# Performance work log

Measured on AMD Instinct MI355X. Metric: run time of the kernel, lower is better.

## Reference

```python
import jax, jax.numpy as jnp
import numpy as np
import math

EMBED = 1024
FF = 4096
HEADS = 16
HEAD = EMBED // HEADS
EPS = 1e-5


def new_gelu(x):
    c = math.sqrt(2.0 / math.pi)
    return 0.5 * x * (1.0 + jnp.tanh(c * (x + 0.044715 * x ** 3)))


def layer_norm(x, g, b):
    mu = jnp.mean(x, axis=-1, keepdims=True)
    var = jnp.var(x, axis=-1, keepdims=True)
    return (x - mu) * jax.lax.rsqrt(var + EPS) * g + b


def setup_inputs() -> dict:
    key = jax.random.key(0)
    ks = jax.random.split(key, 16)
    s = 0.02
    d = {
        'x': jax.random.normal(ks[0], (2, 2048, EMBED), jnp.float32),
        'Wq': jax.random.normal(ks[1], (EMBED, EMBED)) * s,
        'bq': jnp.zeros((EMBED,)),
        'Wk': jax.random.normal(ks[2], (EMBED, EMBED)) * s,
        'bk': jnp.zeros((EMBED,)),
        'Wv': jax.random.normal(ks[3], (EMBED, EMBED)) * s,
        'bv': jnp.zeros((EMBED,)),
        'Wp': jax.random.normal(ks[4], (EMBED, EMBED)) * s,
        'bp': jnp.zeros((EMBED,)),
        'W1': jax.random.normal(ks[5], (EMBED, FF)) * s,
        'b1': jnp.zeros((FF,)),
        'W2': jax.random.normal(ks[6], (FF, EMBED)) * s,
        'b2': jnp.zeros((EMBED,)),
        'g1': jnp.ones((EMBED,)), 'be1': jnp.zeros((EMBED,)),
        'g2': jnp.ones((EMBED,)), 'be2': jnp.zeros((EMBED,)),
    }
    return d


def reference(x, Wq, bq, Wk, bk, Wv, bv, Wp, bp, W1, b1, W2, b2, g1, be1, g2, be2):
    B, S, D = x.shape
    h = layer_norm(x, g1, be1)
    # project and split heads: [B,S,D] -> [B,H,S,Hd]
    def heads(y):
        return y.reshape(B, S, HEADS, HEAD).transpose(0, 2, 1, 3)
    Q = heads(h @ Wq + bq)
    K = heads(h @ Wk + bk)
    V = heads(h @ Wv + bv)
    att = jnp.einsum('bhqd,bhkd->bhqk', Q, K) / math.sqrt(HEAD)
    att = jax.nn.softmax(att, axis=-1)
    out = jnp.einsum('bhqk,bhkd->bhqd', att, V)
    out = out.transpose(0, 2, 1, 3).reshape(B, S, D)
    x = x + (out @ Wp + bp)  # dropout p=0 / eval -> identity
    h2 = layer_norm(x, g2, be2)
    x = x + (new_gelu(h2 @ W1 + b1) @ W2 + b2)
    return x
```

## Files before the change

### kernel.cpp

```cpp
#include <hip/hip_runtime.h>
#include <cstdint>


typedef __attribute__((ext_vector_type(8))) short short8;
typedef __attribute__((ext_vector_type(4))) float f32x4;

__device__ __forceinline__ float bf2f(unsigned short u) {
    union { unsigned int i; float f; } v; v.i = ((unsigned int)u) << 16; return v.f;
}
__device__ __forceinline__ unsigned short f2bf(float f) {
    union { float f; unsigned int i; } v; v.f = f;
    unsigned int u = v.i;
    u += 0x7fff + ((u >> 16) & 1);
    return (unsigned short)(u >> 16);
}
__device__ __forceinline__ float gelu_f(float x) {
    float u = 0.7978845608028654f * (x + 0.044715f * x * x * x);
    float t = 1.f - 2.f / (__expf(2.f * u) + 1.f);
    return 0.5f * x * (1.f + t);
}
__device__ __forceinline__ void async16(const unsigned short* gp, unsigned short* lp) {
    __builtin_amdgcn_global_load_lds(
        (__attribute__((address_space(1))) void*)(gp),
        (__attribute__((address_space(3))) void*)(lp),
        16, 0, 0);
}

__device__ __forceinline__ void ln_dev(
    const float* __restrict__ x, const float* __restrict__ g,
    const float* __restrict__ b, unsigned short* __restrict__ o,
    int row, float* red)
{
    const int tid = threadIdx.x;
    const float4 v = ((const float4*)(x + (size_t)row * 1024))[tid];
    float f0 = v.x, f1 = v.y, f2 = v.z, f3 = v.w;
    float sum = f0 + f1 + f2 + f3;
    float sq  = f0 * f0 + f1 * f1 + f2 * f2 + f3 * f3;
    for (int off = 1; off < 64; off <<= 1) {
        sum += __shfl_xor(sum, off);
        sq  += __shfl_xor(sq,  off);
    }
    int wv = tid >> 6, ln = tid & 63;
    if (ln == 0) { red[wv] = sum; red[4 + wv] = sq; }
    __syncthreads();
    sum = red[0] + red[1] + red[2] + red[3];
    sq  = red[4] + red[5] + red[6] + red[7];
    float mu  = sum * (1.0f / 1024.0f);
    float var = sq  * (1.0f / 1024.0f) - mu * mu;
    float rsd = rsqrtf(fmaxf(var, 0.f) + 1e-5f);
    const float4 gg = ((const float4*)g)[tid];
    const float4 bb = ((const float4*)b)[tid];
    unsigned short* orow = o + (size_t)row * 1024;
    orow[4 * tid + 0] = f2bf((f0 - mu) * rsd * gg.x + bb.x);
    orow[4 * tid + 1] = f2bf((f1 - mu) * rsd * gg.y + bb.y);
    orow[4 * tid + 2] = f2bf((f2 - mu) * rsd * gg.z + bb.z);
    orow[4 * tid + 3] = f2bf((f3 - mu) * rsd * gg.w + bb.w);
}

__device__ __forceinline__ void transpose_dev(
    const float* __restrict__ in, unsigned short* __restrict__ out,
    int R, int C, int inStride, int bx, int by, unsigned short* tile )
{
    const int tx = threadIdx.x & 15, ty = threadIdx.x >> 4;
    const int c0 = bx * 64, r0 = by * 64;
#pragma unroll
    for (int i = 0; i < 4; ++i) {
        int r = ty + 16 * i;
        float4 v = *(const float4*)(in + (size_t)(r0 + r) * inStride + c0 + tx * 4);
        tile[r * 70 + tx * 4 + 0] = f2bf(v.x);
        tile[r * 70 + tx * 4 + 1] = f2bf(v.y);
        tile[r * 70 + tx * 4 + 2] = f2bf(v.z);
        tile[r * 70 + tx * 4 + 3] = f2bf(v.w);
    }
    __syncthreads();
#pragma unroll
    for (int i = 0; i < 4; ++i) {
        int c = ty * 4 + i;
        ushort4 o;
        o.x = tile[(tx * 4 + 0) * 70 + c];
        o.y = tile[(tx * 4 + 1) * 70 + c];
        o.z = tile[(tx * 4 + 2) * 70 + c];
        o.w = tile[(tx * 4 + 3) * 70 + c];
        *(ushort4*)(out + (size_t)(c0 + c) * R + r0 + tx * 4) = o;
    }
}

__global__ __launch_bounds__(256) void ln_k(
    const float* __restrict__ x, const float* __restrict__ g,
    const float* __restrict__ b, unsigned short* __restrict__ o)
{
    __shared__ float red[8];
    ln_dev(x, g, b, o, blockIdx.x, red);
}
__global__ __launch_bounds__(256) void transpose_f2b(
    const float* __restrict__ in, unsigned short* __restrict__ out,
    int R, int C, int inStride)
{
    __shared__ unsigned short tile[64 * 70];
    transpose_dev(in, out, R, C, inStride, blockIdx.x, blockIdx.y, tile);
}
__global__ __launch_bounds__(256) void bcat_k(
    const float* __restrict__ a, const float* __restrict__ b,
    const float* __restrict__ c, float* __restrict__ dst)
{
    int i = blockIdx.x * 256 + threadIdx.x;
    float v = (i < 1024) ? a[i] : (i < 2048) ? b[i - 1024] : c[i - 2048];
    dst[i] = v;
}

__global__ __launch_bounds__(256) void prep1_k(
    const float* __restrict__ x,
    const float* __restrict__ g1, const float* __restrict__ be1,
    const float* __restrict__ Wq, const float* __restrict__ Wk,
    const float* __restrict__ Wv,
    const float* __restrict__ bq, const float* __restrict__ bk,
    const float* __restrict__ bv,
    unsigned short* __restrict__ hb,
    unsigned short* __restrict__ WTqkv,
    float* __restrict__ bcat)
{
    __shared__ unsigned short smem[64 * 70];
    const int b = blockIdx.x;
    if (b < 4096) {
        ln_dev(x, g1, be1, hb, b, (float*)smem);
    } else if (b < 4096 + 768) {
        int t = b - 4096;
        int w = t >> 8;
        int tt = t & 255;
        const float* W = (w == 0) ? Wq : (w == 1) ? Wk : Wv;
        transpose_dev(W, WTqkv + (size_t)w * 1024 * 1024,
                      1024, 1024, 1024, tt & 15, tt >> 4, smem);
    } else {
        int i = (b - 4096 - 768) * 256 + threadIdx.x;
        float v = (i < 1024) ? bq[i] : (i < 2048) ? bk[i - 1024] : bv[i - 2048];
        bcat[i] = v;
    }
}

__global__ __launch_bounds__(256) void prep2_k(
    const float* __restrict__ x1,
    const float* __restrict__ g2, const float* __restrict__ be2,
    const float* __restrict__ W1, const float* __restrict__ W2,
    unsigned short* __restrict__ h2,
    unsigned short* __restrict__ WT1,
    unsigned short* __restrict__ WT2)
{
    __shared__ unsigned short smem[64 * 70];
    const int b = blockIdx.x;
    if (b < 4096) {
        ln_dev(x1, g2, be2, h2, b, (float*)smem);
    } else if (b < 4096 + 1024) {
        int t = b - 4096;
        transpose_dev(W1, WT1, 1024, 4096, 4096, t & 63, t >> 6, smem);
    } else {
        int t = b - 4096 - 1024;
        transpose_dev(W2, WT2, 4096, 1024, 1024, t & 15, t >> 4, smem);
    }
}

__global__ __launch_bounds__(256) void vt_k(
    const unsigned short* __restrict__ src, int stride,
    unsigned short* __restrict__ Vt)
{
    __shared__ unsigned short tile[64][70];
    const int tx = threadIdx.x & 15, ty = threadIdx.x >> 4;
    const int t0 = blockIdx.x * 64;
    const int bh = blockIdx.y;
    const int bo = (bh >> 4) * 2048;
    const int ho = (bh & 15) * 64;
    const unsigned short* s = src + (size_t)bo * stride + ho;
#pragma unroll
    for (int i = 0; i < 4; ++i) {
        int r = ty + 16 * i;
        ushort4 v = *(const ushort4*)(s + (size_t)(t0 + r) * stride + tx * 4);
        tile[r][tx * 4 + 0] = v.x;
        tile[r][tx * 4 + 1] = v.y;
        tile[r][tx * 4 + 2] = v.z;
        tile[r][tx * 4 + 3] = v.w;
    }
    __syncthreads();
    unsigned short* dst = Vt + (size_t)bh * 64 * 2048;
#pragma unroll
    for (int i = 0; i < 4; ++i) {
        int d = ty * 4 + i;
        ushort4 o;
        o.x = tile[tx * 4 + 0][d];
        o.y = tile[tx * 4 + 1][d];
        o.z = tile[tx * 4 + 2][d];
        o.w = tile[tx * 4 + 3][d];
        *(ushort4*)(dst + (size_t)d * 2048 + t0 + tx * 4) = o;
    }
}

__global__ __launch_bounds__(256, 2) void gemm_bt(
    const unsigned short* __restrict__ A,
    const unsigned short* __restrict__ Bt,
    const float* __restrict__ bias,
    const float* __restrict__ res,
    void* __restrict__ C,
    int M, int N, int K, int ldb, int dogelu, int out32)
{
    __shared__ unsigned short sA[2 * 128 * 32];
    __shared__ unsigned short sB[2 * 128 * 32];
    const int tid  = threadIdx.x;
    const int wave = tid >> 6;
    const int lane = tid & 63;
    const int quad = lane >> 4;
    const int l15  = lane & 15;
    const int bm = blockIdx.y * 128;
    const int bn = blockIdx.x * 128;
    const int wM = (wave >> 1) * 64;
    const int wN = (wave & 1) * 64;

    f32x4 acc[4][4];
#pragma unroll
    for (int i = 0; i < 4; ++i)
#pragma unroll
        for (int j = 0; j < 4; ++j)
            acc[i][j] = (f32x4){0.f, 0.f, 0.f, 0.f};

    const int rowS = tid >> 2;
    const int kcS  = (tid & 3) * 8;
    const unsigned short* gA  = A  + (size_t)(bm + rowS) * K + kcS;
    const unsigned short* gA2 = gA + (size_t)64 * K;
    const unsigned short* gB  = Bt + (size_t)(bn + rowS) * ldb + kcS;
    const unsigned short* gB2 = gB + (size_t)64 * ldb;
    unsigned short* lA  = sA + tid * 8;
    unsigned short* lA2 = lA + 64 * 32;
    unsigned short* lB  = sB + tid * 8;
    unsigned short* lB2 = lB + 64 * 32;

    for (int k0 = 0; k0 < K; k0 += 64) {
        __syncthreads();
        async16(gA + k0,       lA);
        async16(gA2 + k0,      lA2);
        async16(gA + k0 + 32,  lA + 4096);
        async16(gA2 + k0 + 32, lA2 + 4096);
        async16(gB + k0,       lB);
        async16(gB2 + k0,      lB2);
        async16(gB + k0 + 32,  lB + 4096);
        async16(gB2 + k0 + 32, lB2 + 4096);
        __syncthreads();

#pragma unroll
        for (int p = 0; p < 2; ++p) {
            short8 aF[4], bF[4];
#pragma unroll
            for (int mi = 0; mi < 4; ++mi)
                aF[mi] = *(const short8*)(sA + p * 4096 + (wM + mi * 16 + l15) * 32 + quad * 8);
#pragma unroll
            for (int ni = 0; ni < 4; ++ni)
                bF[ni] = *(const short8*)(sB + p * 4096 + (wN + ni * 16 + l15) * 32 + quad * 8);
#pragma unroll
            for (int mi = 0; mi < 4; ++mi)
#pragma unroll
                for (int ni = 0; ni < 4; ++ni)
                    acc[mi][ni] = __builtin_amdgcn_mfma_f32_16x16x32_bf16(
                        aF[mi], bF[ni], acc[mi][ni], 0, 0, 0);
        }
    }

#pragma unroll
    for (int ni = 0; ni < 4; ++ni) {
        int col = bn + wN + ni * 16 + l15;
        float bv = bias ? bias[col] : 0.f;
#pragma unroll
        for (int mi = 0; mi < 4; ++mi) {
            int row = bm + wM + mi * 16 + quad * 4;
#pragma unroll
            for (int r = 0; r < 4; ++r) {
                float v = acc[mi][ni][r] + bv;
                if (dogelu) v = gelu_f(v);
                size_t idx = (size_t)(row + r) * N + col;
                if (res) v += res[idx];
                if (out32) ((float*)C)[idx] = v;
                else       ((unsigned short*)C)[idx] = f2bf(v);
            }
        }
    }
}

__global__ __launch_bounds__(256, 2) void gemm_bt64(
    const unsigned short* __restrict__ A,
    const unsigned short* __restrict__ Bt,
    const float* __restrict__ bias,
    const float* __restrict__ res,
    void* __restrict__ C,
    int M, int N, int K, int ldb, int dogelu, int out32)
{
    __shared__ unsigned short sA[2 * 128 * 32];
    __shared__ unsigned short sB[2 * 64 * 32];
    const int tid  = threadIdx.x;
    const int wave = tid >> 6;
    const int lane = tid & 63;
    const int quad = lane >> 4;
    const int l15  = lane & 15;
    const int bm = blockIdx.y * 128;
    const int bn = blockIdx.x * 64;
    const int wM = wave * 32;

    f32x4 acc[2][4];
#pragma unroll
    for (int i = 0; i < 2; ++i)
#pragma unroll
        for (int j = 0; j < 4; ++j)
            acc[i][j] = (f32x4){0.f, 0.f, 0.f, 0.f};

    const int rowS = tid >> 2;
    const int kcS  = (tid & 3) * 8;
    const unsigned short* gA  = A  + (size_t)(bm + rowS) * K + kcS;
    const unsigned short* gA2 = gA + (size_t)64 * K;
    const unsigned short* gB  = Bt + (size_t)(bn + rowS) * ldb + kcS;
    unsigned short* lA  = sA + tid * 8;
    unsigned short* lA2 = lA + 64 * 32;
    unsigned short* lB  = sB + tid * 8;

    for (int k0 = 0; k0 < K; k0 += 64) {
        __syncthreads();
        async16(gA + k0,       lA);
        async16(gA2 + k0,      lA2);
        async16(gA + k0 + 32,  lA + 4096);
        async16(gA2 + k0 + 32, lA2 + 4096);
        async16(gB + k0,       lB);
        async16(gB + k0 + 32,  lB + 2048);
        __syncthreads();

#pragma unroll
        for (int p = 0; p < 2; ++p) {
            short8 aF[2], bF[4];
#pragma unroll
            for (int mi = 0; mi < 2; ++mi)
                aF[mi] = *(const short8*)(sA + p * 4096 + (wM + mi * 16 + l15) * 32 + quad * 8);
#pragma unroll
            for (int ni = 0; ni < 4; ++ni)
                bF[ni] = *(const short8*)(sB + p * 2048 + (ni * 16 + l15) * 32 + quad * 8);
#pragma unroll
            for (int mi = 0; mi < 2; ++mi)
#pragma unroll
                for (int ni = 0; ni < 4; ++ni)
                    acc[mi][ni] = __builtin_amdgcn_mfma_f32_16x16x32_bf16(
                        aF[mi], bF[ni], acc[mi][ni], 0, 0, 0);
        }
    }

#pragma unroll
    for (int ni = 0; ni < 4; ++ni) {
        int col = bn + ni * 16 + l15;
        float bv = bias ? bias[col] : 0.f;
#pragma unroll
        for (int mi = 0; mi < 2; ++mi) {
            int row = bm + wM + mi * 16 + quad * 4;
#pragma unroll
            for (int r = 0; r < 4; ++r) {
                float v = acc[mi][ni][r] + bv;
                if (dogelu) v = gelu_f(v);
                size_t idx = (size_t)(row + r) * N + col;
                if (res) v += res[idx];
                if (out32) ((float*)C)[idx] = v;
                else       ((unsigned short*)C)[idx] = f2bf(v);
            }
        }
    }
}

__global__ __launch_bounds__(256, 2) void attn_k(
    const unsigned short* __restrict__ Q,
    const unsigned short* __restrict__ K,
    const unsigned short* __restrict__ Vt,
    unsigned short* __restrict__ O, int qs)
{
    __shared__ unsigned short sQ [128 * 88];
    __shared__ unsigned short sKP[128 * 88];
    __shared__ unsigned short sVt[64 * 88];

    const int tid  = threadIdx.x;
    const int wave = tid >> 6;
    const int lane = tid & 63;
    const int quad = lane >> 4;
    const int l15  = lane & 15;
    const int qb = blockIdx.x * 128;
    const int bh = blockIdx.y;
    const int bo = (bh >> 4) * 2048;
    const int ho = (bh & 15) * 64;

    const unsigned short* Qb  = Q  + (size_t)bo * qs + ho;
    const unsigned short* Kb  = K  + (size_t)bo * qs + ho;
    const unsigned short* Vtb = Vt + (size_t)bh * 64 * 2048;

    const int rowS = tid >> 3;
    const int dcS  = (tid & 7) * 8;

#pragma unroll
    for (int r = 0; r < 4; ++r) {
        int row = r * 32 + rowS;
        short8 v = *(const short8*)(Qb + (size_t)(qb + row) * qs + dcS);
        *(short8*)(sQ + row * 88 + dcS) = v;
    }

    short8 onesF;
#pragma unroll
    for (int j = 0; j < 8; ++j) onesF[j] = (short)0x3F80;

    f32x4 accO[2][4];
    f32x4 accL[2];
#pragma unroll
    for (int mi = 0; mi < 2; ++mi) {
        accL[mi] = (f32x4){0.f, 0.f, 0.f, 0.f};
#pragma unroll
        for (int nd = 0; nd < 4; ++nd) accO[mi][nd] = (f32x4){0.f, 0.f, 0.f, 0.f};
    }

    for (int kt = 0; kt < 2048; kt += 64) {
        __syncthreads();
#pragma unroll
        for (int r = 0; r < 2; ++r) {
            int row = r * 32 + rowS;
            short8 kv = *(const short8*)(Kb + (size_t)(kt + row) * qs + dcS);
            *(short8*)(sKP + row * 88 + dcS) = kv;
            short8 vv = *(const short8*)(Vtb + (size_t)row * 2048 + kt + dcS);
            *(short8*)(sVt + row * 88 + dcS) = vv;
        }
        __syncthreads();

        f32x4 accS[2][4];
#pragma unroll
        for (int mi = 0; mi < 2; ++mi)
#pragma unroll
            for (int ni = 0; ni < 4; ++ni) accS[mi][ni] = (f32x4){0.f, 0.f, 0.f, 0.f};
#pragma unroll
        for (int ks = 0; ks < 2; ++ks) {
            short8 aQ[2], bK[4];
#pragma unroll
            for (int mi = 0; mi < 2; ++mi)
                aQ[mi] = *(const short8*)(sQ + (wave * 32 + mi * 16 + l15) * 88 + ks * 32 + quad * 8);
#pragma unroll
            for (int ni = 0; ni < 4; ++ni)
                bK[ni] = *(const short8*)(sKP + (ni * 16 + l15) * 88 + ks * 32 + quad * 8);
#pragma unroll
            for (int mi = 0; mi < 2; ++mi)
#pragma unroll
                for (int ni = 0; ni < 4; ++ni)
                    accS[mi][ni] = __builtin_amdgcn_mfma_f32_16x16x32_bf16(
                        aQ[mi], bK[ni], accS[mi][ni], 0, 0, 0);
        }
        __syncthreads();

#pragma unroll
        for (int mi = 0; mi < 2; ++mi) {
            int prow = wave * 32 + mi * 16 + quad * 4;
#pragma unroll
            for (int r = 0; r < 4; ++r) {
                float p0 = __expf(accS[mi][0][r] * 0.125f);
                float p1 = __expf(accS[mi][1][r] * 0.125f);
                float p2 = __expf(accS[mi][2][r] * 0.125f);
                float p3 = __expf(accS[mi][3][r] * 0.125f);
                sKP[(prow + r) * 88 +      l15] = f2bf(p0);
                sKP[(prow + r) * 88 + 16 + l15] = f2bf(p1);
                sKP[(prow + r) * 88 + 32 + l15] = f2bf(p2);
                sKP[(prow + r) * 88 + 48 + l15] = f2bf(p3);
            }
        }

#pragma unroll
        for (int ks = 0; ks < 2; ++ks) {
            short8 aP[2], bV[4];
#pragma unroll
            for (int mi = 0; mi < 2; ++mi)
                aP[mi] = *(const short8*)(sKP + (wave * 32 + mi * 16 + l15) * 88 + ks * 32 + quad * 8);
#pragma unroll
            for (int nd = 0; nd < 4; ++nd)
                bV[nd] = *(const short8*)(sVt + (nd * 16 + l15) * 88 + ks * 32 + quad * 8);
#pragma unroll
            for (int mi = 0; mi < 2; ++mi) {
#pragma unroll
                for (int nd = 0; nd < 4; ++nd)
                    accO[mi][nd] = __builtin_amdgcn_mfma_f32_16x16x32_bf16(
                        aP[mi], bV[nd], accO[mi][nd], 0, 0, 0);
                accL[mi] = __builtin_amdgcn_mfma_f32_16x16x32_bf16(
                    aP[mi], onesF, accL[mi], 0, 0, 0);
            }
        }
    }

#pragma unroll
    for (int mi = 0; mi < 2; ++mi)
#pragma unroll
        for (int r = 0; r < 4; ++r) {
            int row = qb + wave * 32 + mi * 16 + quad * 4 + r;
            float inv = 1.f / accL[mi][r];
#pragma unroll
            for (int nd = 0; nd < 4; ++nd)
                O[(size_t)(bo + row) * 1024 + ho + nd * 16 + l15] =
                    f2bf(accO[mi][nd][r] * inv);
        }
}

extern "C" void kernel_launch(void* const* d_in, const int* in_sizes, int n_in,
                              void* d_out, int out_size, void* d_ws, size_t ws_size,
                              hipStream_t stream)
{
    (void)in_sizes; (void)n_in; (void)out_size;
    const float* x   = (const float*)d_in[0];
    const float* Wq  = (const float*)d_in[1];
    const float* bq  = (const float*)d_in[2];
    const float* Wk  = (const float*)d_in[3];
    const float* bk  = (const float*)d_in[4];
    const float* Wv  = (const float*)d_in[5];
    const float* bv  = (const float*)d_in[6];
    const float* Wp  = (const float*)d_in[7];
    const float* bp  = (const float*)d_in[8];
    const float* W1  = (const float*)d_in[9];
    const float* b1  = (const float*)d_in[10];
    const float* W2  = (const float*)d_in[11];
    const float* b2  = (const float*)d_in[12];
    const float* g1  = (const float*)d_in[13];
    const float* be1 = (const float*)d_in[14];
    const float* g2  = (const float*)d_in[15];
    const float* be2 = (const float*)d_in[16];
    float* out = (float*)d_out;

    char* ws = (char*)d_ws;
    char* dob = (char*)d_out;
    const size_t MB = 1024 * 1024;

    if (ws_size >= 40 * MB) {
        unsigned short* hb    = (unsigned short*)dob;
        unsigned short* WTqkv = (unsigned short*)(dob + 8 * MB);
        float*          bcat  = (float*)(dob + 14 * MB);
        unsigned short* QKV   = (unsigned short*)ws;
        unsigned short* att   = (unsigned short*)(ws + 24 * MB);
        unsigned short* Vt    = (unsigned short*)(ws + 32 * MB);
        unsigned short* WTp   = (unsigned short*)(ws + 32 * MB);
        unsigned short* h2    = (unsigned short*)ws;
        unsigned short* WT1   = (unsigned short*)(ws + 8 * MB);
        unsigned short* WT2   = (unsigned short*)(ws + 16 * MB);
        unsigned short* act   = (unsigned short*)(ws + 24 * MB);

        prep1_k<<<4096 + 768 + 12, 256, 0, stream>>>(
            x, g1, be1, Wq, Wk, Wv, bq, bk, bv, hb, WTqkv, bcat);
        gemm_bt<<<dim3(24, 32), 256, 0, stream>>>(hb, WTqkv, bcat, nullptr, QKV,
                                                  4096, 3072, 1024, 1024, 0, 0);
        vt_k<<<dim3(32, 32), 256, 0, stream>>>(QKV + 2048, 3072, Vt);
        attn_k<<<dim3(16, 32), 256, 0, stream>>>(QKV, QKV + 1024, Vt, att, 3072);
        transpose_f2b<<<dim3(16, 16), 256, 0, stream>>>(Wp, WTp, 1024, 1024, 1024);
        gemm_bt64<<<dim3(16, 32), 256, 0, stream>>>(att, WTp, bp, x, out,
                                                    4096, 1024, 1024, 1024, 0, 1);
        prep2_k<<<4096 + 2048, 256, 0, stream>>>(out, g2, be2, W1, W2, h2, WT1, WT2);
        for (int c = 0; c < 2; ++c) {
            gemm_bt<<<dim3(16, 32), 256, 0, stream>>>(h2, WT1 + (size_t)c * 2048 * 1024,
                                                      b1 + c * 2048, nullptr, act,
                                                      4096, 2048, 1024, 1024, 1, 0);
            gemm_bt64<<<dim3(16, 32), 256, 0, stream>>>(act, WT2 + (size_t)c * 2048,
                                                        c == 0 ? b2 : nullptr, out, out,
                                                        4096, 1024, 2048, 4096, 0, 1);
        }
    } else {
        unsigned short* Qw  = (unsigned short*)(ws);
        unsigned short* Kw  = (unsigned short*)(ws + 8 * MB);
        unsigned short* Vw  = (unsigned short*)(ws + 16 * MB);
        unsigned short* hb  = (unsigned short*)dob;
        unsigned short* WTq = (unsigned short*)(dob + 8 * MB);
        unsigned short* VtF = (unsigned short*)(dob + 8 * MB);
        unsigned short* att = Qw;
        unsigned short* WTb = Kw;
        unsigned short* h2  = Vw;
        unsigned short* act = Qw;

        ln_k<<<4096, 256, 0, stream>>>(x, g1, be1, hb);
        transpose_f2b<<<dim3(16, 16), 256, 0, stream>>>(Wq, WTq, 1024, 1024, 1024);
        gemm_bt<<<dim3(8, 32), 256, 0, stream>>>(hb, WTq, bq, nullptr, Qw, 4096, 1024, 1024, 1024, 0, 0);
        transpose_f2b<<<dim3(16, 16), 256, 0, stream>>>(Wk, WTq, 1024, 1024, 1024);
        gemm_bt<<<dim3(8, 32), 256, 0, stream>>>(hb, WTq, bk, nullptr, Kw, 4096, 1024, 1024, 1024, 0, 0);
        transpose_f2b<<<dim3(16, 16), 256, 0, stream>>>(Wv, WTq, 1024, 1024, 1024);
        gemm_bt<<<dim3(8, 32), 256, 0, stream>>>(hb, WTq, bv, nullptr, Vw, 4096, 1024, 1024, 1024, 0, 0);
        vt_k<<<dim3(32, 32), 256, 0, stream>>>(Vw, 1024, VtF);
        attn_k<<<dim3(16, 32), 256, 0, stream>>>(Qw, Kw, VtF, att, 1024);
        transpose_f2b<<<dim3(16, 16), 256, 0, stream>>>(Wp, WTb, 1024, 1024, 1024);
        gemm_bt64<<<dim3(16, 32), 256, 0, stream>>>(att, WTb, bp, x, out, 4096, 1024, 1024, 1024, 0, 1);
        ln_k<<<4096, 256, 0, stream>>>(out, g2, be2, h2);
        for (int c = 0; c < 4; ++c) {
            transpose_f2b<<<dim3(16, 16), 256, 0, stream>>>(W1 + c * 1024, WTb, 1024, 1024, 4096);
            gemm_bt64<<<dim3(16, 32), 256, 0, stream>>>(h2, WTb, b1 + c * 1024, nullptr, act,
                                                        4096, 1024, 1024, 1024, 1, 0);
            unsigned short* WT2c = WTb + 1024 * 1024;
            transpose_f2b<<<dim3(16, 16), 256, 0, stream>>>(W2 + (size_t)c * 1024 * 1024, WT2c,
                                                            1024, 1024, 1024);
            gemm_bt64<<<dim3(16, 32), 256, 0, stream>>>(act, WT2c, c == 0 ? b2 : nullptr,
                                                        out, out, 4096, 1024, 1024, 1024, 0, 1);
        }
    }
}
```

Before: 399.3 us.

## Restructure attention kernel: register Q, double-buffered K/V, per-wave P tiles

The attention kernel now handles 256 query rows per block with each wave owning 64 rows. Q is kept in registers and K/V tiles are double-buffered in shared memory with register prefetch, which removes one barrier per iteration. Each wave writes P to its own LDS tile using packed bf16 conversion, and the V transpose permutes key order to match the packed P layout. The change also lowers launch bounds to 1 block per SM, halves the grid and raises MFMA priority, trading occupancy and parallelism for less LDS traffic and fewer syncs.

New measurement: 399.3 us. About the same (-0.0%).

```diff
diff --git a/kernel.cpp b/kernel.cpp
--- a/kernel.cpp
+++ b/kernel.cpp
@@ -183,12 +183,12 @@
 #pragma unroll
     for (int i = 0; i < 4; ++i) {
         int d = ty * 4 + i;
-        ushort4 o;
-        o.x = tile[tx * 4 + 0][d];
-        o.y = tile[tx * 4 + 1][d];
-        o.z = tile[tx * 4 + 2][d];
-        o.w = tile[tx * 4 + 3][d];
-        *(ushort4*)(dst + (size_t)d * 2048 + t0 + tx * 4) = o;
+#pragma unroll
+        for (int c = 0; c < 4; ++c) {
+            int t = tx * 4 + c;
+            int sg = (t & 15) * 4 + (t >> 4);
+            dst[(size_t)d * 2048 + t0 + sg] = tile[t][d];
+        }
     }
 }
 
@@ -363,22 +363,22 @@
     }
 }
 
-__global__ __launch_bounds__(256, 2) void attn_k(
+__global__ __launch_bounds__(256, 1) void attn_k(
     const unsigned short* __restrict__ Q,
     const unsigned short* __restrict__ K,
     const unsigned short* __restrict__ Vt,
     unsigned short* __restrict__ O, int qs)
 {
-    __shared__ unsigned short sQ [128 * 88];
-    __shared__ unsigned short sKP[128 * 88];
-    __shared__ unsigned short sVt[64 * 88];
+    __shared__ unsigned short sK[2][64 * 88];
+    __shared__ unsigned short sV[2][64 * 88];
+    __shared__ unsigned short sP[4][64 * 88];
 
     const int tid  = threadIdx.x;
     const int wave = tid >> 6;
     const int lane = tid & 63;
     const int quad = lane >> 4;
     const int l15  = lane & 15;
-    const int qb = blockIdx.x * 128;
+    const int qb = blockIdx.x * 256;
     const int bh = blockIdx.y;
     const int bo = (bh >> 4) * 2048;
     const int ho = (bh & 15) * 64;
@@ -386,107 +386,131 @@
     const unsigned short* Qb  = Q  + (size_t)bo * qs + ho;
     const unsigned short* Kb  = K  + (size_t)bo * qs + ho;
     const unsigned short* Vtb = Vt + (size_t)bh * 64 * 2048;
+    unsigned short* sPw = sP[wave];
+
+    short8 qF[2][4];
+#pragma unroll
+    for (int ks = 0; ks < 2; ++ks)
+#pragma unroll
+        for (int mi = 0; mi < 4; ++mi)
+            qF[ks][mi] = *(const short8*)(Qb +
+                (size_t)(qb + wave * 64 + mi * 16 + l15) * qs + ks * 32 + quad * 8);
+
+    short8 onesF;
+#pragma unroll
+    for (int j = 0; j < 8; ++j) onesF[j] = (short)0x3F80;
+
+    f32x4 accO[4][4];
+    f32x4 accL[4];
+#pragma unroll
+    for (int mi = 0; mi < 4; ++mi) {
+        accL[mi] = (f32x4){0.f, 0.f, 0.f, 0.f};
+#pragma unroll
+        for (int nd = 0; nd < 4; ++nd) accO[mi][nd] = (f32x4){0.f, 0.f, 0.f, 0.f};
+    }
 
     const int rowS = tid >> 3;
     const int dcS  = (tid & 7) * 8;
 
-#pragma unroll
-    for (int r = 0; r < 4; ++r) {
-        int row = r * 32 + rowS;
-        short8 v = *(const short8*)(Qb + (size_t)(qb + row) * qs + dcS);
-        *(short8*)(sQ + row * 88 + dcS) = v;
-    }
-
-    short8 onesF;
-#pragma unroll
-    for (int j = 0; j < 8; ++j) onesF[j] = (short)0x3F80;
-
-    f32x4 accO[2][4];
-    f32x4 accL[2];
-#pragma unroll
-    for (int mi = 0; mi < 2; ++mi) {
-        accL[mi] = (f32x4){0.f, 0.f, 0.f, 0.f};
-#pragma unroll
-        for (int nd = 0; nd < 4; ++nd) accO[mi][nd] = (f32x4){0.f, 0.f, 0.f, 0.f};
+    short8 kr[2], vr[2];
+#pragma unroll
+    for (int r = 0; r < 2; ++r) {
+        kr[r] = *(const short8*)(Kb + (size_t)(r * 32 + rowS) * qs + dcS);
+        vr[r] = *(const short8*)(Vtb + (size_t)(r * 32 + rowS) * 2048 + dcS);
+    }
+#pragma unroll
+    for (int r = 0; r < 2; ++r) {
+        *(short8*)(&sK[0][(r * 32 + rowS) * 88 + dcS]) = kr[r];
+        *(short8*)(&sV[0][(r * 32 + rowS) * 88 + dcS]) = vr[r];
+    }
+#pragma unroll
+    for (int r = 0; r < 2; ++r) {
+        kr[r] = *(const short8*)(Kb + (size_t)(64 + r * 32 + rowS) * qs + dcS);
+        vr[r] = *(const short8*)(Vtb + (size_t)(r * 32 + rowS) * 2048 + 64 + dcS);
     }
 
     for (int kt = 0; kt < 2048; kt += 64) {
+        const int buf = (kt >> 6) & 1;
         __syncthreads();
-#pragma unroll
-        for (int r = 0; r < 2; ++r) {
-            int row = r * 32 + rowS;
-            short8 kv = *(const short8*)(Kb + (size_t)(kt + row) * qs + dcS);
-            *(short8*)(sKP + row * 88 + dcS) = kv;
-            short8 vv = *(const short8*)(Vtb + (size_t)row * 2048 + kt + dcS);
-            *(short8*)(sVt + row * 88 + dcS) = vv;
-        }
-        __syncthreads();
-
-        f32x4 accS[2][4];
-#pragma unroll
-        for (int mi = 0; mi < 2; ++mi)
-#pragma unroll
-            for (int ni = 0; ni < 4; ++ni) accS[mi][ni] = (f32x4){0.f, 0.f, 0.f, 0.f};
-#pragma unroll
-        for (int ks = 0; ks < 2; ++ks) {
-            short8 aQ[2], bK[4];
-#pragma unroll
-            for (int mi = 0; mi < 2; ++mi)
-                aQ[mi] = *(const short8*)(sQ + (wave * 32 + mi * 16 + l15) * 88 + ks * 32 + quad * 8);
+
+        short8 bK[2][4];
+#pragma unroll
+        for (int ks = 0; ks < 2; ++ks)
 #pragma unroll
             for (int ni = 0; ni < 4; ++ni)
-                bK[ni] = *(const short8*)(sKP + (ni * 16 + l15) * 88 + ks * 32 + quad * 8);
-#pragma unroll
-            for (int mi = 0; mi < 2; ++mi)
-#pragma unroll
-                for (int ni = 0; ni < 4; ++ni)
-                    accS[mi][ni] = __builtin_amdgcn_mfma_f32_16x16x32_bf16(
-                        aQ[mi], bK[ni], accS[mi][ni], 0, 0, 0);
-        }
-        __syncthreads();
-
-#pragma unroll
-        for (int mi = 0; mi < 2; ++mi) {
-            int prow = wave * 32 + mi * 16 + quad * 4;
+                bK[ks][ni] = *(const short8*)(&sK[buf][(ni * 16 + l15) * 88 + ks * 32 + quad * 8]);
+
+#pragma unroll
+        for (int mi = 0; mi < 4; ++mi) {
+            f32x4 s0 = (f32x4){0.f, 0.f, 0.f, 0.f};
+            f32x4 s1 = s0, s2 = s0, s3 = s0;
+#pragma unroll
+            for (int ks = 0; ks < 2; ++ks) {
+                s0 = __builtin_amdgcn_mfma_f32_16x16x32_bf16(qF[ks][mi], bK[ks][0], s0, 0, 0, 0);
+                s1 = __builtin_amdgcn_mfma_f32_16x16x32_bf16(qF[ks][mi], bK[ks][1], s1, 0, 0, 0);
+                s2 = __builtin_amdgcn_mfma_f32_16x16x32_bf16(qF[ks][mi], bK[ks][2], s2, 0, 0, 0);
+                s3 = __builtin_amdgcn_mfma_f32_16x16x32_bf16(qF[ks][mi], bK[ks][3], s3, 0, 0, 0);
+            }
 #pragma unroll
             for (int r = 0; r < 4; ++r) {
-                float p0 = __expf(accS[mi][0][r] * 0.125f);
-                float p1 = __expf(accS[mi][1][r] * 0.125f);
-                float p2 = __expf(accS[mi][2][r] * 0.125f);
-                float p3 = __expf(accS[mi][3][r] * 0.125f);
-                sKP[(prow + r) * 88 +      l15] = f2bf(p0);
-                sKP[(prow + r) * 88 + 16 + l15] = f2bf(p1);
-                sKP[(prow + r) * 88 + 32 + l15] = f2bf(p2);
-                sKP[(prow + r) * 88 + 48 + l15] = f2bf(p3);
+                float p0 = __expf(s0[r] * 0.125f);
+                float p1 = __expf(s1[r] * 0.125f);
+                float p2 = __expf(s2[r] * 0.125f);
+                float p3 = __expf(s3[r] * 0.125f);
+                unsigned int w0, w1;
+                asm("v_cvt_pk_bf16_f32 %0, %1, %2" : "=v"(w0) : "v"(p0), "v"(p1));
+                asm("v_cvt_pk_bf16_f32 %0, %1, %2" : "=v"(w1) : "v"(p2), "v"(p3));
+                uint2 w; w.x = w0; w.y = w1;
+                *(uint2*)(&sPw[(mi * 16 + quad * 4 + r) * 88 + l15 * 4]) = w;
             }
         }
 
-#pragma unroll
-        for (int ks = 0; ks < 2; ++ks) {
-            short8 aP[2], bV[4];
-#pragma unroll
-            for (int mi = 0; mi < 2; ++mi)
-                aP[mi] = *(const short8*)(sKP + (wave * 32 + mi * 16 + l15) * 88 + ks * 32 + quad * 8);
+        if (kt + 64 < 2048) {
+            const int nb = buf ^ 1;
+#pragma unroll
+            for (int r = 0; r < 2; ++r) {
+                *(short8*)(&sK[nb][(r * 32 + rowS) * 88 + dcS]) = kr[r];
+                *(short8*)(&sV[nb][(r * 32 + rowS) * 88 + dcS]) = vr[r];
+            }
+            if (kt + 128 < 2048) {
+#pragma unroll
+                for (int r = 0; r < 2; ++r) {
+                    kr[r] = *(const short8*)(Kb + (size_t)(kt + 128 + r * 32 + rowS) * qs + dcS);
+                    vr[r] = *(const short8*)(Vtb + (size_t)(r * 32 + rowS) * 2048 + kt + 128 + dcS);
+                }
+            }
+        }
+
+        short8 bV[2][4];
+#pragma unroll
+        for (int ks = 0; ks < 2; ++ks)
 #pragma unroll
             for (int nd = 0; nd < 4; ++nd)
-                bV[nd] = *(const short8*)(sVt + (nd * 16 + l15) * 88 + ks * 32 + quad * 8);
-#pragma unroll
-            for (int mi = 0; mi < 2; ++mi) {
-#pragma unroll
-                for (int nd = 0; nd < 4; ++nd)
-                    accO[mi][nd] = __builtin_amdgcn_mfma_f32_16x16x32_bf16(
-                        aP[mi], bV[nd], accO[mi][nd], 0, 0, 0);
-                accL[mi] = __builtin_amdgcn_mfma_f32_16x16x32_bf16(
-                    aP[mi], onesF, accL[mi], 0, 0, 0);
+                bV[ks][nd] = *(const short8*)(&sV[buf][(nd * 16 + l15) * 88 + ks * 32 + quad * 8]);
+
+        __builtin_amdgcn_s_setprio(1);
+#pragma unroll
+        for (int mi = 0; mi < 4; ++mi) {
+            short8 aP0 = *(const short8*)(&sPw[(mi * 16 + l15) * 88 + quad * 8]);
+            short8 aP1 = *(const short8*)(&sPw[(mi * 16 + l15) * 88 + 32 + quad * 8]);
+#pragma unroll
+            for (int nd = 0; nd < 4; ++nd) {
+                accO[mi][nd] = __builtin_amdgcn_mfma_f32_16x16x32_bf16(
+                    aP0, bV[0][nd], accO[mi][nd], 0, 0, 0);
+                accO[mi][nd] = __builtin_amdgcn_mfma_f32_16x16x32_bf16(
+                    aP1, bV[1][nd], accO[mi][nd], 0, 0, 0);
             }
-        }
-    }
-
-#pragma unroll
-    for (int mi = 0; mi < 2; ++mi)
+            accL[mi] = __builtin_amdgcn_mfma_f32_16x16x32_bf16(aP0, onesF, accL[mi], 0, 0, 0);
+            accL[mi] = __builtin_amdgcn_mfma_f32_16x16x32_bf16(aP1, onesF, accL[mi], 0, 0, 0);
+        }
+        __builtin_amdgcn_s_setprio(0);
+    }
+
+#pragma unroll
+    for (int mi = 0; mi < 4; ++mi)
 #pragma unroll
         for (int r = 0; r < 4; ++r) {
-            int row = qb + wave * 32 + mi * 16 + quad * 4 + r;
+            int row = qb + wave * 64 + mi * 16 + quad * 4 + r;
             float inv = 1.f / accL[mi][r];
 #pragma unroll
             for (int nd = 0; nd < 4; ++nd)
@@ -541,7 +565,7 @@
         gemm_bt<<<dim3(24, 32), 256, 0, stream>>>(hb, WTqkv, bcat, nullptr, QKV,
                                                   4096, 3072, 1024, 1024, 0, 0);
         vt_k<<<dim3(32, 32), 256, 0, stream>>>(QKV + 2048, 3072, Vt);
-        attn_k<<<dim3(16, 32), 256, 0, stream>>>(QKV, QKV + 1024, Vt, att, 3072);
+        attn_k<<<dim3(8, 32), 256, 0, stream>>>(QKV, QKV + 1024, Vt, att, 3072);
         transpose_f2b<<<dim3(16, 16), 256, 0, stream>>>(Wp, WTp, 1024, 1024, 1024);
         gemm_bt64<<<dim3(16, 32), 256, 0, stream>>>(att, WTp, bp, x, out,
                                                     4096, 1024, 1024, 1024, 0, 1);
@@ -574,7 +598,7 @@
         transpose_f2b<<<dim3(16, 16), 256, 0, stream>>>(Wv, WTq, 1024, 1024, 1024);
         gemm_bt<<<dim3(8, 32), 256, 0, stream>>>(hb, WTq, bv, nullptr, Vw, 4096, 1024, 1024, 1024, 0, 0);
         vt_k<<<dim3(32, 32), 256, 0, stream>>>(Vw, 1024, VtF);
-        attn_k<<<dim3(16, 32), 256, 0, stream>>>(Qw, Kw, VtF, att, 1024);
+        attn_k<<<dim3(8, 32), 256, 0, stream>>>(Qw, Kw, VtF, att, 1024);
         transpose_f2b<<<dim3(16, 16), 256, 0, stream>>>(Wp, WTb, 1024, 1024, 1024);
         gemm_bt64<<<dim3(16, 32), 256, 0, stream>>>(att, WTb, bp, x, out, 4096, 1024, 1024, 1024, 0, 1);
         ln_k<<<4096, 256, 0, stream>>>(out, g2, be2, h2);
```
